# Kernel tuning notes

Measured on AMD Instinct MI355X. Metric: run time of the kernel, lower is better.

Reference implementation:

```python
import jax, jax.numpy as jnp
import numpy as np

H = 512  # h_dim = d_rnn


def _pair_mlp(paragraph, W1, W2):
    """Fused equivalent of: cat(p_i, p_j) @ W1 -> ReLU -> @ W2 -> ReLU.
    Splits W1 so the [B,n,n,2h] concatenated input is never materialized
    before the first GEMM.  paragraph: [B, n, H]; W1: [2H, 2H]; W2: [2H, d_pair].
    Returns [B, n, n, d_pair].
    """
    u = paragraph @ W1[:H]   # [B, n, 2H]  (contribution of p_i, broadcast over j)
    v = paragraph @ W1[H:]   # [B, n, 2H]  (contribution of p_j, broadcast over i)
    z = jax.nn.relu(u[:, :, None, :] + v[:, None, :, :])  # [B, n, n, 2H]
    return jax.nn.relu(z @ W2)  # [B, n, n, d_pair]  (dropout = identity in eval)


def reference(paragraph, Wf1, Wf2, w3, Wh1a, Wh1b, wl1, Wh2a, Wh2b, wl2):
    # rela_encode -> future MLP, then directional probs via w3
    rela_vec = _pair_mlp(paragraph, Wf1, Wf2)            # [B,n,n,d_pair]
    rela_p = jax.nn.softmax(rela_vec @ w3, axis=-1)      # [B,n,n,2]
    rela_vec_diret = jnp.concatenate((rela_vec, rela_p), axis=-1)

    # encode_history -> hist_left1 / hist_left2 MLPs and their heads
    hist1 = _pair_mlp(paragraph, Wh1a, Wh1b)
    hist2 = _pair_mlp(paragraph, Wh2a, Wh2b)
    left1_p = jax.nn.softmax(hist1 @ wl1, axis=-1)
    left2_p = jax.nn.softmax(hist2 @ wl2, axis=-1)
    hist_vec_left1 = jnp.concatenate((hist1, left1_p), axis=-1)
    hist_vec_left2 = jnp.concatenate((hist2, left2_p), axis=-1)

    # pack all rela_pred outputs into one tensor: [B, n, n, 3*(d_pair+2)]
    return jnp.concatenate((rela_vec_diret, hist_vec_left1, hist_vec_left2), axis=-1)


def setup_inputs() -> dict:
    key = jax.random.key(0)
    ks = jax.random.split(key, 10)
    B, N, d_pair = 4, 128, 256
    s1 = 1.0 / np.sqrt(2 * H)
    s2 = 1.0 / np.sqrt(d_pair)
    return {
        "paragraph": jax.random.normal(ks[0], (B, N, H), jnp.float32),
        "Wf1": jax.random.normal(ks[1], (2 * H, 2 * H), jnp.float32) * s1,
        "Wf2": jax.random.normal(ks[2], (2 * H, d_pair), jnp.float32) * s1,
        "w3": jax.random.normal(ks[3], (d_pair, 2), jnp.float32) * s2,
        "Wh1a": jax.random.normal(ks[4], (2 * H, 2 * H), jnp.float32) * s1,
        "Wh1b": jax.random.normal(ks[5], (2 * H, d_pair), jnp.float32) * s1,
        "wl1": jax.random.normal(ks[6], (d_pair, 2), jnp.float32) * s2,
        "Wh2a": jax.random.normal(ks[7], (2 * H, 2 * H), jnp.float32) * s1,
        "Wh2b": jax.random.normal(ks[8], (2 * H, d_pair), jnp.float32) * s1,
        "wl2": jax.random.normal(ks[9], (d_pair, 2), jnp.float32) * s2,
    }
```

## Files before the change

### kernel.cpp

```cpp
#include <hip/hip_runtime.h>


typedef __attribute__((ext_vector_type(4))) float floatx4;
typedef __attribute__((ext_vector_type(2))) float floatx2;
typedef __attribute__((ext_vector_type(8))) short short8;

#define KT 16
#define LSTRIDE 68

__device__ __forceinline__ void gload_lds16(const void* g, void* l) {
  __builtin_amdgcn_global_load_lds(
      (const __attribute__((address_space(1))) void*)g,
      (__attribute__((address_space(3))) void*)l, 16, 0, 0);
}

__global__ __launch_bounds__(256) void stage1_valu(
    const float* __restrict__ P,
    const float* __restrict__ W1,
    float* __restrict__ uv) {
  __shared__ float at[KT][LSTRIDE];
  __shared__ float wt[KT][LSTRIDE];
  int bx = blockIdx.x;
  int m0 = (bx >> 5) * 64;
  int c0 = (bx & 31) * 64;
  int half = c0 >> 10;
  int ccol = c0 & 1023;
  int tid = threadIdx.x;
  int tm = tid >> 4, tn = tid & 15;
  int lm = tid >> 2;
  int lk4 = (tid & 3) * 4;
  int lkk = tid >> 4;
  int lc4 = (tid & 15) * 4;

  float acc[4][4] = {};

  for (int k0 = 0; k0 < 512; k0 += KT) {
    floatx4 pa = *(const floatx4*)(P + (long)(m0 + lm) * 512 + k0 + lk4);
    floatx4 wa = *(const floatx4*)(W1 + (long)(half * 512 + k0 + lkk) * 1024 + ccol + lc4);
    __syncthreads();
#pragma unroll
    for (int e = 0; e < 4; e++) at[lk4 + e][lm] = pa[e];
    *(floatx4*)&wt[lkk][lc4] = wa;
    __syncthreads();
#pragma unroll
    for (int kk = 0; kk < KT; kk++) {
      floatx4 av = *(const floatx4*)&at[kk][tm * 4];
      floatx4 wv = *(const floatx4*)&wt[kk][tn * 4];
#pragma unroll
      for (int mm = 0; mm < 4; mm++)
#pragma unroll
        for (int nn = 0; nn < 4; nn++)
          acc[mm][nn] += av[mm] * wv[nn];
    }
  }
#pragma unroll
  for (int mm = 0; mm < 4; mm++) {
    floatx4 o;
#pragma unroll
    for (int nn = 0; nn < 4; nn++) o[nn] = acc[mm][nn];
    *(floatx4*)(uv + (long)(m0 + tm * 4 + mm) * 2048 + c0 + tn * 4) = o;
  }
}

__global__ __launch_bounds__(256) void prep_w2(
    const float* __restrict__ W2,
    unsigned short* __restrict__ W2F) {
  int t = blockIdx.x * 256 + threadIdx.x;
  int lane = t & 63;
  int nf = (t >> 6) & 15;
  int kt = t >> 10;
  int g = lane >> 4, c = lane & 15;
  int n = nf * 16 + c;
  int kbase = kt * 32 + g * 8;

  union U { unsigned u[4]; short8 s; };
  U H, L;
  unsigned hb[8], lb[8];
#pragma unroll
  for (int e = 0; e < 8; e++) {
    float w = W2[(long)(kbase + e) * 256 + n];
    unsigned wb = __float_as_uint(w);
    unsigned h = wb & 0xFFFF0000u;
    float l = w - __uint_as_float(h);
    hb[e] = h;
    lb[e] = __float_as_uint(l) & 0xFFFF0000u;
  }
#pragma unroll
  for (int p = 0; p < 4; p++) {
    H.u[p] = __builtin_amdgcn_perm(hb[2 * p + 1], hb[2 * p], 0x07060302u);
    L.u[p] = __builtin_amdgcn_perm(lb[2 * p + 1], lb[2 * p], 0x07060302u);
  }
  long base = (((long)kt * 16 + nf) * 2) * 64 + lane;
  *(short8*)(W2F + (base + 0) * 8) = H.s;
  *(short8*)(W2F + (base + 64) * 8) = L.s;
}

__device__ __forceinline__ void make_frag(
    const floatx4& ua, const floatx4& ub,
    const floatx4& va, const floatx4& vb,
    short8& hi, short8& lo) {
  unsigned hb[8], lb[8];
#pragma unroll
  for (int e = 0; e < 8; e++) {
    float z = (e < 4) ? (ua[e] + va[e]) : (ub[e - 4] + vb[e - 4]);
    z = fmaxf(z, 0.0f);
    unsigned zb = __float_as_uint(z);
    unsigned h = zb & 0xFFFF0000u;
    float l = z - __uint_as_float(h);
    hb[e] = h;
    lb[e] = __float_as_uint(l) & 0xFFFF0000u;
  }
  union U { unsigned u[4]; short8 s; };
  U H, L;
#pragma unroll
  for (int p = 0; p < 4; p++) {
    H.u[p] = __builtin_amdgcn_perm(hb[2 * p + 1], hb[2 * p], 0x07060302u);
    L.u[p] = __builtin_amdgcn_perm(lb[2 * p + 1], lb[2 * p], 0x07060302u);
  }
  hi = H.s;
  lo = L.s;
}

__global__ __launch_bounds__(256, 2) void pair_mfma(
    const float* __restrict__ uv,
    const unsigned short* __restrict__ W2F,
    const float* __restrict__ w3,
    float* __restrict__ out, int mlp) {
  __shared__ unsigned short wbuf[2][16384];
  int bi = blockIdx.x;
  int b = bi >> 7;
  int tid = threadIdx.x;
  int wid = tid >> 6;
  int lane = tid & 63;
  int g = lane >> 4;
  int r = lane & 15;
  int wj = wid * 32;

  const float* ubase = uv + (long)bi * 2048;
  const float* v0 = uv + (long)(b * 128 + wj + r) * 2048 + 1024;
  const float* v1 = v0 + 16 * 2048;

  floatx4 acc[2][16];
#pragma unroll
  for (int mm = 0; mm < 2; mm++)
#pragma unroll
    for (int nf = 0; nf < 16; nf++) acc[mm][nf] = (floatx4){0.f, 0.f, 0.f, 0.f};

  {
    const unsigned short* gs = W2F;
#pragma unroll
    for (int i = 0; i < 8; i++)
      gload_lds16(gs + (i * 256 + wid * 64 + lane) * 8,
                  &wbuf[0][(i * 256 + wid * 64) * 8]);
  }
  __syncthreads();

  int cur = 0;
  for (int kt = 0; kt < 32; kt++) {
    if (kt < 31) {
      const unsigned short* gs = W2F + (long)(kt + 1) * 16384;
#pragma unroll
      for (int i = 0; i < 8; i++)
        gload_lds16(gs + (i * 256 + wid * 64 + lane) * 8,
                    &wbuf[cur ^ 1][(i * 256 + wid * 64) * 8]);
    }

    int k0 = kt * 32 + g * 8;
    floatx4 u0  = *(const floatx4*)(ubase + k0);
    floatx4 u1  = *(const floatx4*)(ubase + k0 + 4);
    floatx4 va0 = *(const floatx4*)(v0 + k0);
    floatx4 va1 = *(const floatx4*)(v0 + k0 + 4);
    floatx4 vb0 = *(const floatx4*)(v1 + k0);
    floatx4 vb1 = *(const floatx4*)(v1 + k0 + 4);

    short8 ahi[2], alo[2];
    make_frag(u0, u1, va0, va1, ahi[0], alo[0]);
    make_frag(u0, u1, vb0, vb1, ahi[1], alo[1]);

    const unsigned short* wf = &wbuf[cur][lane * 8];
#pragma unroll
    for (int nf = 0; nf < 16; nf++) {
      short8 whi = *(const short8*)(wf + (nf * 2 + 0) * 512);
      short8 wlo = *(const short8*)(wf + (nf * 2 + 1) * 512);
#pragma unroll
      for (int mm = 0; mm < 2; mm++) {
        acc[mm][nf] = __builtin_amdgcn_mfma_f32_16x16x32_bf16(
            ahi[mm], whi, acc[mm][nf], 0, 0, 0);
        acc[mm][nf] = __builtin_amdgcn_mfma_f32_16x16x32_bf16(
            alo[mm], whi, acc[mm][nf], 0, 0, 0);
        acc[mm][nf] = __builtin_amdgcn_mfma_f32_16x16x32_bf16(
            ahi[mm], wlo, acc[mm][nf], 0, 0, 0);
      }
    }
    __syncthreads();
    cur ^= 1;
  }

  float* ob = out + (long)(bi * 128) * 774 + mlp * 258;
  floatx2 w3v[16];
#pragma unroll
  for (int nf = 0; nf < 16; nf++)
    w3v[nf] = *(const floatx2*)(w3 + (nf * 16 + r) * 2);
#pragma unroll
  for (int mm = 0; mm < 2; mm++) {
    int jrow = wj + mm * 16 + g * 4;
#pragma unroll
    for (int reg = 0; reg < 4; reg++) {
      float* orow = ob + (long)(jrow + reg) * 774;
      float s0 = 0.f, s1 = 0.f;
#pragma unroll
      for (int nf = 0; nf < 16; nf++) {
        float y = acc[mm][nf][reg];
        y = y > 0.f ? y : 0.f;
        orow[nf * 16 + r] = y;
        s0 += y * w3v[nf][0];
        s1 += y * w3v[nf][1];
      }
#pragma unroll
      for (int off = 1; off < 16; off <<= 1) {
        s0 += __shfl_xor(s0, off, 64);
        s1 += __shfl_xor(s1, off, 64);
      }
      if (r == 0) {
        float m = fmaxf(s0, s1);
        float e0 = __expf(s0 - m), e1 = __expf(s1 - m);
        float inv = 1.0f / (e0 + e1);
        floatx2 pr;
        pr[0] = e0 * inv;
        pr[1] = e1 * inv;
        *(floatx2*)(orow + 256) = pr;
      }
    }
  }
}

__global__ __launch_bounds__(256) void pair_valu(
    const float* __restrict__ uv,
    const float* __restrict__ W2,
    float* __restrict__ out, int mlp) {
  __shared__ float zt[KT][LSTRIDE];
  __shared__ float wt[KT][LSTRIDE];
  int bx = blockIdx.x;
  int nb = bx & 3;
  int jh = (bx >> 2) & 1;
  int bi = bx >> 3;
  int b = bi >> 7;
  int j0 = jh * 64;
  int n0 = nb * 64;
  int tid = threadIdx.x;
  int tm = tid >> 4, tn = tid & 15;
  int lj = tid >> 2;
  int lk4 = (tid & 3) * 4;
  int lkk = tid >> 4;
  int ln4 = (tid & 15) * 4;

  const float* urow = uv + (long)bi * 2048;
  const float* vrow = uv + (long)(b * 128 + j0 + lj) * 2048 + 1024;

  float acc[4][4] = {};

  for (int k0 = 0; k0 < 1024; k0 += KT) {
    floatx4 uu = *(const floatx4*)(urow + k0 + lk4);
    floatx4 vv = *(const floatx4*)(vrow + k0 + lk4);
    floatx4 wa = *(const floatx4*)(W2 + (long)(k0 + lkk) * 256 + n0 + ln4);
    __syncthreads();
#pragma unroll
    for (int e = 0; e < 4; e++) {
      float z = uu[e] + vv[e];
      zt[lk4 + e][lj] = z > 0.f ? z : 0.f;
    }
    *(floatx4*)&wt[lkk][ln4] = wa;
    __syncthreads();
#pragma unroll
    for (int kk = 0; kk < KT; kk++) {
      floatx4 zv = *(const floatx4*)&zt[kk][tm * 4];
      floatx4 wv = *(const floatx4*)&wt[kk][tn * 4];
#pragma unroll
      for (int mm = 0; mm < 4; mm++)
#pragma unroll
        for (int nn = 0; nn < 4; nn++)
          acc[mm][nn] += zv[mm] * wv[nn];
    }
  }
  float* ob = out + (long)(bi * 128 + j0) * 774 + mlp * 258 + n0 + tn * 4;
#pragma unroll
  for (int mm = 0; mm < 4; mm++) {
    float* orow = ob + (long)(tm * 4 + mm) * 774;
    floatx2 pa, pb;
    pa[0] = acc[mm][0] > 0.f ? acc[mm][0] : 0.f;
    pa[1] = acc[mm][1] > 0.f ? acc[mm][1] : 0.f;
    pb[0] = acc[mm][2] > 0.f ? acc[mm][2] : 0.f;
    pb[1] = acc[mm][3] > 0.f ? acc[mm][3] : 0.f;
    *(floatx2*)orow = pa;
    *(floatx2*)(orow + 2) = pb;
  }
}

__global__ __launch_bounds__(256) void head_kernel(
    const float* __restrict__ w3_0, const float* __restrict__ w3_1,
    const float* __restrict__ w3_2, float* out) {
  int wid = threadIdx.x >> 6, lane = threadIdx.x & 63;
  int r = blockIdx.x * 4 + wid;
  int mlp = r >> 16;
  int row = r & 65535;
  const float* w3 = (mlp == 0) ? w3_0 : (mlp == 1) ? w3_1 : w3_2;
  const float* yp = out + (long)row * 774 + mlp * 258 + lane * 4;
  floatx2 ya = *(const floatx2*)yp;
  floatx2 yb = *(const floatx2*)(yp + 2);
  const float* wp = w3 + lane * 8;
  floatx4 wv0 = *(const floatx4*)wp;
  floatx4 wv1 = *(const floatx4*)(wp + 4);
  float s0 = ya[0] * wv0[0] + ya[1] * wv0[2] + yb[0] * wv1[0] + yb[1] * wv1[2];
  float s1 = ya[0] * wv0[1] + ya[1] * wv0[3] + yb[0] * wv1[1] + yb[1] * wv1[3];
#pragma unroll
  for (int off = 32; off > 0; off >>= 1) {
    s0 += __shfl_xor(s0, off, 64);
    s1 += __shfl_xor(s1, off, 64);
  }
  if (lane == 0) {
    float m = fmaxf(s0, s1);
    float e0 = __expf(s0 - m), e1 = __expf(s1 - m);
    float inv = 1.0f / (e0 + e1);
    floatx2 pr;
    pr[0] = e0 * inv;
    pr[1] = e1 * inv;
    *(floatx2*)(out + (long)row * 774 + mlp * 258 + 256) = pr;
  }
}

extern "C" void kernel_launch(void* const* d_in, const int* in_sizes, int n_in,
                              void* d_out, int out_size, void* d_ws, size_t ws_size,
                              hipStream_t stream) {
  const float* para = (const float*)d_in[0];
  const float* Wf1  = (const float*)d_in[1];
  const float* Wf2  = (const float*)d_in[2];
  const float* w3   = (const float*)d_in[3];
  const float* Wh1a = (const float*)d_in[4];
  const float* Wh1b = (const float*)d_in[5];
  const float* wl1  = (const float*)d_in[6];
  const float* Wh2a = (const float*)d_in[7];
  const float* Wh2b = (const float*)d_in[8];
  const float* wl2  = (const float*)d_in[9];

  float* uv = (float*)d_ws;
  unsigned short* w2f =
      (unsigned short*)((char*)d_ws + (4u << 20));
  float* outp = (float*)d_out;

  bool mfma_ok = ws_size >= (size_t)(5u << 20);

  const float* W1s[3] = {Wf1, Wh1a, Wh2a};
  const float* W2s[3] = {Wf2, Wh1b, Wh2b};
  const float* w3s[3] = {w3, wl1, wl2};
  for (int mlp = 0; mlp < 3; mlp++) {
    stage1_valu<<<256, 256, 0, stream>>>(para, W1s[mlp], uv);
    if (mfma_ok) {
      prep_w2<<<128, 256, 0, stream>>>(W2s[mlp], w2f);
      pair_mfma<<<512, 256, 0, stream>>>(uv, w2f, w3s[mlp], outp, mlp);
    } else {
      pair_valu<<<4096, 256, 0, stream>>>(uv, W2s[mlp], outp, mlp);
    }
  }
  if (!mfma_ok) head_kernel<<<49152, 256, 0, stream>>>(w3, wl1, wl2, outp);
}
```

Baseline: 580.2 us.

## Move stage-1 GEMM to split-bf16 MFMA and split pair_mfma N across waves

Replaces the fp32 VALU stage-1 projection with a pre-packed hi/lo bf16 MFMA kernel, so the per-MLP W1 is converted to fragment layout once per launch. The pair kernel moves to 512 threads with each wave computing half of the output columns. This halves accumulator registers per wave and raises occupancy. The two halves' softmax partial sums are combined through LDS after a barrier. Stage-1 MFMA runs only when the workspace is at least 9 MB, and it adds an extra prep kernel per MLP.

```diff
diff --git a/kernel.cpp b/kernel.cpp
--- a/kernel.cpp
+++ b/kernel.cpp
@@ -12,6 +12,106 @@
   __builtin_amdgcn_global_load_lds(
       (const __attribute__((address_space(1))) void*)g,
       (__attribute__((address_space(3))) void*)l, 16, 0, 0);
+}
+
+__device__ __forceinline__ void split8(const float* x, short8& hi, short8& lo) {
+  unsigned hb[8], lb[8];
+#pragma unroll
+  for (int e = 0; e < 8; e++) {
+    unsigned xb = __float_as_uint(x[e]);
+    unsigned h = xb & 0xFFFF0000u;
+    float l = x[e] - __uint_as_float(h);
+    hb[e] = h;
+    lb[e] = __float_as_uint(l) & 0xFFFF0000u;
+  }
+  union U { unsigned u[4]; short8 s; };
+  U H, L;
+#pragma unroll
+  for (int p = 0; p < 4; p++) {
+    H.u[p] = __builtin_amdgcn_perm(hb[2 * p + 1], hb[2 * p], 0x07060302u);
+    L.u[p] = __builtin_amdgcn_perm(lb[2 * p + 1], lb[2 * p], 0x07060302u);
+  }
+  hi = H.s;
+  lo = L.s;
+}
+
+__global__ __launch_bounds__(256) void prep_w1f(
+    const float* __restrict__ W1,
+    unsigned short* __restrict__ W1F) {
+  int t = blockIdx.x * 256 + threadIdx.x;
+  int lane = t & 63;
+  int nf = (t >> 6) & 127;
+  int kt = t >> 13;
+  int g = lane >> 4, c = lane & 15;
+  int n = nf * 16 + c;
+  int kbase = kt * 32 + g * 8;
+  const float* src = W1 + (long)((n >= 1024 ? 512 : 0) + kbase) * 1024 + (n & 1023);
+
+  unsigned hb[8], lb[8];
+#pragma unroll
+  for (int e = 0; e < 8; e++) {
+    float w = src[(long)e * 1024];
+    unsigned wb = __float_as_uint(w);
+    unsigned h = wb & 0xFFFF0000u;
+    float l = w - __uint_as_float(h);
+    hb[e] = h;
+    lb[e] = __float_as_uint(l) & 0xFFFF0000u;
+  }
+  union U { unsigned u[4]; short8 s; };
+  U H, L;
+#pragma unroll
+  for (int p = 0; p < 4; p++) {
+    H.u[p] = __builtin_amdgcn_perm(hb[2 * p + 1], hb[2 * p], 0x07060302u);
+    L.u[p] = __builtin_amdgcn_perm(lb[2 * p + 1], lb[2 * p], 0x07060302u);
+  }
+  long base = ((long)kt * 128 + nf) * 2 * 64 + lane;
+  *(short8*)(W1F + (base + 0) * 8) = H.s;
+  *(short8*)(W1F + (base + 64) * 8) = L.s;
+}
+
+__global__ __launch_bounds__(256) void stage1_mfma(
+    const float* __restrict__ P,
+    const unsigned short* __restrict__ W1F,
+    float* __restrict__ uv) {
+  int bx = blockIdx.x;
+  int m0 = (bx >> 4) * 16;
+  int n0 = (bx & 15) * 128;
+  int tid = threadIdx.x;
+  int wid = tid >> 6, lane = tid & 63;
+  int g = lane >> 4, r = lane & 15;
+  int nw0 = n0 + wid * 32;
+
+  const float* prow = P + (long)(m0 + r) * 512;
+
+  floatx4 acc[2];
+#pragma unroll
+  for (int nf = 0; nf < 2; nf++) acc[nf] = (floatx4){0.f, 0.f, 0.f, 0.f};
+
+  for (int kt = 0; kt < 16; kt++) {
+    int k0 = kt * 32 + g * 8;
+    float a[8];
+    floatx4 a0 = *(const floatx4*)(prow + k0);
+    floatx4 a1 = *(const floatx4*)(prow + k0 + 4);
+#pragma unroll
+    for (int e = 0; e < 4; e++) { a[e] = a0[e]; a[4 + e] = a1[e]; }
+    short8 ahi, alo;
+    split8(a, ahi, alo);
+#pragma unroll
+    for (int nf = 0; nf < 2; nf++) {
+      int nfg = (nw0 >> 4) + nf;
+      const unsigned short* wp = W1F + (((long)kt * 128 + nfg) * 2 * 64 + lane) * 8;
+      short8 whi = *(const short8*)wp;
+      short8 wlo = *(const short8*)(wp + 64 * 8);
+      acc[nf] = __builtin_amdgcn_mfma_f32_16x16x32_bf16(ahi, whi, acc[nf], 0, 0, 0);
+      acc[nf] = __builtin_amdgcn_mfma_f32_16x16x32_bf16(alo, whi, acc[nf], 0, 0, 0);
+      acc[nf] = __builtin_amdgcn_mfma_f32_16x16x32_bf16(ahi, wlo, acc[nf], 0, 0, 0);
+    }
+  }
+#pragma unroll
+  for (int nf = 0; nf < 2; nf++)
+#pragma unroll
+    for (int reg = 0; reg < 4; reg++)
+      uv[(long)(m0 + g * 4 + reg) * 2048 + nw0 + nf * 16 + r] = acc[nf][reg];
 }
 
 __global__ __launch_bounds__(256) void stage1_valu(
@@ -73,8 +173,6 @@
   int n = nf * 16 + c;
   int kbase = kt * 32 + g * 8;
 
-  union U { unsigned u[4]; short8 s; };
-  U H, L;
   unsigned hb[8], lb[8];
 #pragma unroll
   for (int e = 0; e < 8; e++) {
@@ -85,6 +183,8 @@
     hb[e] = h;
     lb[e] = __float_as_uint(l) & 0xFFFF0000u;
   }
+  union U { unsigned u[4]; short8 s; };
+  U H, L;
 #pragma unroll
   for (int p = 0; p < 4; p++) {
     H.u[p] = __builtin_amdgcn_perm(hb[2 * p + 1], hb[2 * p], 0x07060302u);
@@ -99,29 +199,16 @@
     const floatx4& ua, const floatx4& ub,
     const floatx4& va, const floatx4& vb,
     short8& hi, short8& lo) {
-  unsigned hb[8], lb[8];
-#pragma unroll
-  for (int e = 0; e < 8; e++) {
-    float z = (e < 4) ? (ua[e] + va[e]) : (ub[e - 4] + vb[e - 4]);
-    z = fmaxf(z, 0.0f);
-    unsigned zb = __float_as_uint(z);
-    unsigned h = zb & 0xFFFF0000u;
-    float l = z - __uint_as_float(h);
-    hb[e] = h;
-    lb[e] = __float_as_uint(l) & 0xFFFF0000u;
-  }
-  union U { unsigned u[4]; short8 s; };
-  U H, L;
-#pragma unroll
-  for (int p = 0; p < 4; p++) {
-    H.u[p] = __builtin_amdgcn_perm(hb[2 * p + 1], hb[2 * p], 0x07060302u);
-    L.u[p] = __builtin_amdgcn_perm(lb[2 * p + 1], lb[2 * p], 0x07060302u);
-  }
-  hi = H.s;
-  lo = L.s;
-}
-
-__global__ __launch_bounds__(256, 2) void pair_mfma(
+  float z[8];
+#pragma unroll
+  for (int e = 0; e < 4; e++) {
+    z[e] = fmaxf(ua[e] + va[e], 0.0f);
+    z[4 + e] = fmaxf(ub[e] + vb[e], 0.0f);
+  }
+  split8(z, hi, lo);
+}
+
+__global__ __launch_bounds__(512, 4) void pair_mfma(
     const float* __restrict__ uv,
     const unsigned short* __restrict__ W2F,
     const float* __restrict__ w3,
@@ -132,27 +219,25 @@
   int tid = threadIdx.x;
   int wid = tid >> 6;
   int lane = tid & 63;
+  int jq = wid >> 1;
+  int nh = wid & 1;
   int g = lane >> 4;
   int r = lane & 15;
-  int wj = wid * 32;
+  int wj = jq * 32;
 
   const float* ubase = uv + (long)bi * 2048;
   const float* v0 = uv + (long)(b * 128 + wj + r) * 2048 + 1024;
   const float* v1 = v0 + 16 * 2048;
 
-  floatx4 acc[2][16];
+  floatx4 acc[2][8];
 #pragma unroll
   for (int mm = 0; mm < 2; mm++)
 #pragma unroll
-    for (int nf = 0; nf < 16; nf++) acc[mm][nf] = (floatx4){0.f, 0.f, 0.f, 0.f};
-
-  {
-    const unsigned short* gs = W2F;
-#pragma unroll
-    for (int i = 0; i < 8; i++)
-      gload_lds16(gs + (i * 256 + wid * 64 + lane) * 8,
-                  &wbuf[0][(i * 256 + wid * 64) * 8]);
-  }
+    for (int nf = 0; nf < 8; nf++) acc[mm][nf] = (floatx4){0.f, 0.f, 0.f, 0.f};
+
+#pragma unroll
+  for (int i = 0; i < 4; i++)
+    gload_lds16(W2F + (i * 512 + tid) * 8, &wbuf[0][(i * 512 + tid) * 8]);
   __syncthreads();
 
   int cur = 0;
@@ -160,9 +245,8 @@
     if (kt < 31) {
       const unsigned short* gs = W2F + (long)(kt + 1) * 16384;
 #pragma unroll
-      for (int i = 0; i < 8; i++)
-        gload_lds16(gs + (i * 256 + wid * 64 + lane) * 8,
-                    &wbuf[cur ^ 1][(i * 256 + wid * 64) * 8]);
+      for (int i = 0; i < 4; i++)
+        gload_lds16(gs + (i * 512 + tid) * 8, &wbuf[cur ^ 1][(i * 512 + tid) * 8]);
     }
 
     int k0 = kt * 32 + g * 8;
@@ -177,11 +261,12 @@
     make_frag(u0, u1, va0, va1, ahi[0], alo[0]);
     make_frag(u0, u1, vb0, vb1, ahi[1], alo[1]);
 
-    const unsigned short* wf = &wbuf[cur][lane * 8];
-#pragma unroll
-    for (int nf = 0; nf < 16; nf++) {
-      short8 whi = *(const short8*)(wf + (nf * 2 + 0) * 512);
-      short8 wlo = *(const short8*)(wf + (nf * 2 + 1) * 512);
+#pragma unroll
+    for (int nf = 0; nf < 8; nf++) {
+      int nfg = nh * 8 + nf;
+      const unsigned short* wp = &wbuf[cur][(nfg * 2) * 512 + lane * 8];
+      short8 whi = *(const short8*)wp;
+      short8 wlo = *(const short8*)(wp + 512);
 #pragma unroll
       for (int mm = 0; mm < 2; mm++) {
         acc[mm][nf] = __builtin_amdgcn_mfma_f32_16x16x32_bf16(
@@ -196,20 +281,21 @@
     cur ^= 1;
   }
 
+  float* ps = (float*)wbuf;
   float* ob = out + (long)(bi * 128) * 774 + mlp * 258;
-  floatx2 w3v[16];
-#pragma unroll
-  for (int nf = 0; nf < 16; nf++)
-    w3v[nf] = *(const floatx2*)(w3 + (nf * 16 + r) * 2);
+  floatx2 w3v[8];
+#pragma unroll
+  for (int nf = 0; nf < 8; nf++)
+    w3v[nf] = *(const floatx2*)(w3 + ((nh * 8 + nf) * 16 + r) * 2);
 #pragma unroll
   for (int mm = 0; mm < 2; mm++) {
     int jrow = wj + mm * 16 + g * 4;
 #pragma unroll
     for (int reg = 0; reg < 4; reg++) {
-      float* orow = ob + (long)(jrow + reg) * 774;
+      float* orow = ob + (long)(jrow + reg) * 774 + nh * 128;
       float s0 = 0.f, s1 = 0.f;
 #pragma unroll
-      for (int nf = 0; nf < 16; nf++) {
+      for (int nf = 0; nf < 8; nf++) {
         float y = acc[mm][nf][reg];
         y = y > 0.f ? y : 0.f;
         orow[nf * 16 + r] = y;
@@ -222,15 +308,24 @@
         s1 += __shfl_xor(s1, off, 64);
       }
       if (r == 0) {
-        float m = fmaxf(s0, s1);
-        float e0 = __expf(s0 - m), e1 = __expf(s1 - m);
-        float inv = 1.0f / (e0 + e1);
-        floatx2 pr;
-        pr[0] = e0 * inv;
-        pr[1] = e1 * inv;
-        *(floatx2*)(orow + 256) = pr;
+        int row = jrow + reg;
+        ps[(row * 2 + nh) * 2 + 0] = s0;
+        ps[(row * 2 + nh) * 2 + 1] = s1;
       }
     }
+  }
+  __syncthreads();
+  if (nh == 1 && lane < 32) {
+    int row = wj + lane;
+    float s0 = ps[(row * 2) * 2 + 0] + ps[(row * 2 + 1) * 2 + 0];
+    float s1 = ps[(row * 2) * 2 + 1] + ps[(row * 2 + 1) * 2 + 1];
+    float m = fmaxf(s0, s1);
+    float e0 = __expf(s0 - m), e1 = __expf(s1 - m);
+    float inv = 1.0f / (e0 + e1);
+    floatx2 pr;
+    pr[0] = e0 * inv;
+    pr[1] = e1 * inv;
+    *(floatx2*)(ob + (long)row * 774 + 256) = pr;
   }
 }
 
@@ -345,21 +440,29 @@
   float* uv = (float*)d_ws;
   unsigned short* w2f =
       (unsigned short*)((char*)d_ws + (4u << 20));
+  unsigned short* w1f =
+      (unsigned short*)((char*)d_ws + (5u << 20));
   float* outp = (float*)d_out;
 
-  bool mfma_ok = ws_size >= (size_t)(5u << 20);
+  bool pair_ok   = ws_size >= (size_t)(5u << 20);
+  bool stage1_ok = ws_size >= (size_t)(9u << 20);
 
   const float* W1s[3] = {Wf1, Wh1a, Wh2a};
   const float* W2s[3] = {Wf2, Wh1b, Wh2b};
   const float* w3s[3] = {w3, wl1, wl2};
   for (int mlp = 0; mlp < 3; mlp++) {
-    stage1_valu<<<256, 256, 0, stream>>>(para, W1s[mlp], uv);
-    if (mfma_ok) {
+    if (stage1_ok) {
+      prep_w1f<<<512, 256, 0, stream>>>(W1s[mlp], w1f);
+      stage1_mfma<<<512, 256, 0, stream>>>(para, w1f, uv);
+    } else {
+      stage1_valu<<<256, 256, 0, stream>>>(para, W1s[mlp], uv);
+    }
+    if (pair_ok) {
       prep_w2<<<128, 256, 0, stream>>>(W2s[mlp], w2f);
-      pair_mfma<<<512, 256, 0, stream>>>(uv, w2f, w3s[mlp], outp, mlp);
+      pair_mfma<<<512, 512, 0, stream>>>(uv, w2f, w3s[mlp], outp, mlp);
     } else {
       pair_valu<<<4096, 256, 0, stream>>>(uv, W2s[mlp], outp, mlp);
     }
   }
-  if (!mfma_ok) head_kernel<<<49152, 256, 0, stream>>>(w3, wl1, wl2, outp);
-}
+  if (!pair_ok) head_kernel<<<49152, 256, 0, stream>>>(w3, wl1, wl2, outp);
+}
```

New measurement: 545.2 us. -6.0%, faster.
